# Performance work log

Measured on AMD Instinct MI355X. Metric: run time of the kernel, lower is better.

The kernel has to match this reference:

```python
import jax, jax.numpy as jnp
import numpy as np

B, T = 512, 200
N_SKILLS, M, DK, DV, H = 1000, 50, 64, 64, 128


def setup_inputs() -> dict:
    key = jax.random.key(0)
    ks = jax.random.split(key, 12)
    inp = {
        'skill_seq': jax.random.randint(ks[0], (B, T), 0, N_SKILLS, dtype=jnp.int32),
        'correct_seq': jax.random.randint(ks[1], (B, T), 0, 2, dtype=jnp.int32),
        'mask': jnp.ones((B, T), dtype=jnp.float32),
        'skill_embed': jax.random.normal(ks[2], (N_SKILLS, DK), dtype=jnp.float32),
        'key_memory': jax.random.normal(ks[3], (M, DK), dtype=jnp.float32) * 0.1,
        'value_init': jnp.zeros((M, DV), dtype=jnp.float32),
        'interaction_embed': jax.random.normal(ks[4], (2 * N_SKILLS, DV), dtype=jnp.float32),
        'erase_W': jax.random.normal(ks[5], (DV, DV), dtype=jnp.float32) * 0.05,
        'erase_b': jnp.zeros((DV,), dtype=jnp.float32),
        'add_W': jax.random.normal(ks[6], (DV, DV), dtype=jnp.float32) * 0.05,
        'add_b': jnp.zeros((DV,), dtype=jnp.float32),
        'fc1_W': jax.random.normal(ks[7], (DK + DV, H), dtype=jnp.float32) * 0.05,
        'fc1_b': jnp.zeros((H,), dtype=jnp.float32),
        'fc2_W': jax.random.normal(ks[8], (H, 1), dtype=jnp.float32) * 0.05,
        'fc2_b': jnp.zeros((1,), dtype=jnp.float32),
    }
    return inp


def reference(skill_seq, correct_seq, mask, skill_embed, key_memory, value_init,
              interaction_embed, erase_W, erase_b, add_W, add_b,
              fc1_W, fc1_b, fc2_W, fc2_b):
    n_skills = skill_embed.shape[0]
    b = skill_seq.shape[0]
    # Time-invariant-per-step quantities are precomputed vectorized over (B,T):
    q = skill_embed[skill_seq]                                   # (B,T,dk)
    w = jax.nn.softmax(jnp.einsum('btk,mk->btm', q, key_memory), axis=-1)  # (B,T,M)
    v = interaction_embed[skill_seq + correct_seq * n_skills]    # (B,T,dv)
    e = jax.nn.sigmoid(v @ erase_W + erase_b)                    # (B,T,dv)
    a = jnp.tanh(v @ add_W + add_b)                              # (B,T,dv)

    def step(mem, inputs):
        # mem: (B,M,dv); read BEFORE write, matching the torch loop
        w_t, e_t, a_t = inputs                                   # (B,M),(B,dv),(B,dv)
        read = jnp.einsum('bm,bmv->bv', w_t, mem)                # (B,dv)
        we = w_t[:, :, None]                                     # (B,M,1)
        mem = mem * (1.0 - we * e_t[:, None, :]) + we * a_t[:, None, :]
        return mem, read

    mem0 = jnp.broadcast_to(value_init, (b,) + value_init.shape)
    _, reads = jax.lax.scan(step, mem0,
                            (jnp.swapaxes(w, 0, 1), jnp.swapaxes(e, 0, 1), jnp.swapaxes(a, 0, 1)))
    reads = jnp.swapaxes(reads, 0, 1)                            # (B,T,dv)

    x = jnp.concatenate([q, reads], axis=-1)                     # (B,T,dk+dv)
    h = jax.nn.relu(x @ fc1_W + fc1_b)
    logit = (h @ fc2_W + fc2_b)[..., 0]
    p = jax.nn.sigmoid(logit)
    return p * mask, correct_seq.astype(jnp.float32) * mask
```

## Files before the change

kernel.cpp:

```cpp
#include <hip/hip_runtime.h>
#include <hip/hip_bf16.h>

#define B_  512
#define T_  200
#define NS  1000
#define M_  50
#define DK  64
#define DV  64
#define H_  128
#define NPOS (B_ * T_)

typedef __hip_bfloat16 bf16;
typedef unsigned short ushort_t;
typedef __bf16 bf16x8 __attribute__((ext_vector_type(8)));
typedef float  f32x4  __attribute__((ext_vector_type(4)));

__device__ __forceinline__ float ldf(const void* p, int i, int isbf) {
    return isbf ? __bfloat162float(((const bf16*)p)[i]) : ((const float*)p)[i];
}
__device__ __forceinline__ int sniff(const void* mask) {
    return (*(const unsigned*)mask == 0x3F800000u) ? 0 : 1;
}
__device__ __forceinline__ float rl(float x, int l) {
    return __int_as_float(__builtin_amdgcn_readlane(__float_as_int(x), l));
}
__device__ __forceinline__ ushort_t f2bf(float v) {
    bf16 h = __float2bfloat16(v);
    return *(ushort_t*)&h;
}

__global__ __launch_bounds__(256) void dk21_tabs(
    const void* __restrict__ mask,
    const void* __restrict__ skill_embed, const void* __restrict__ key_memory,
    const void* __restrict__ inter,
    const void* __restrict__ eW, const void* __restrict__ eb,
    const void* __restrict__ aW, const void* __restrict__ ab,
    const void* __restrict__ fc1W, const void* __restrict__ fc1b,
    float* __restrict__ w_tab, unsigned* __restrict__ ea_tab,
    float* __restrict__ hq_tab, ushort_t* __restrict__ W2f) {
    int isbf = sniff(mask);
    int lane = threadIdx.x & 63;
    int gwid = (blockIdx.x << 2) | (threadIdx.x >> 6);

    if (gwid < NS) {
        int s = gwid;
        int kq = lane >> 4, r = lane & 15;
        int row = 13 * kq + r;
        int valid = (r < 13) && (row < M_);
        float q = ldf(skill_embed, s * DK + lane, isbf);
        float acc = 0.f;
        if (valid) {
            #pragma unroll 16
            for (int k = 0; k < DK; ++k)
                acc = fmaf(rl(q, k), ldf(key_memory, row * DK + k, isbf), acc);
        }
        float val = valid ? acc : -1e30f;
        float mx = val;
        #pragma unroll
        for (int off = 1; off < 64; off <<= 1) mx = fmaxf(mx, __shfl_xor(mx, off, 64));
        float ex = valid ? __expf(val - mx) : 0.f;
        float sm = ex;
        #pragma unroll
        for (int off = 1; off < 64; off <<= 1) sm += __shfl_xor(sm, off, 64);
        w_tab[s * 64 + lane] = valid ? ex / sm : 0.f;
    } else if (gwid < 3 * NS) {
        int r = gwid - NS;
        float vv = ldf(inter, r * DV + lane, isbf);
        float eacc = ldf(eb, lane, isbf);
        float aacc = ldf(ab, lane, isbf);
        #pragma unroll 16
        for (int u = 0; u < DV; ++u) {
            float vu = rl(vv, u);
            eacc = fmaf(vu, ldf(eW, u * DV + lane, isbf), eacc);
            aacc = fmaf(vu, ldf(aW, u * DV + lane, isbf), aacc);
        }
        float ev = 1.f / (1.f + __expf(-eacc));
        float av = tanhf(aacc);
        ea_tab[r * 64 + lane] = ((unsigned)f2bf(av) << 16) | (unsigned)f2bf(ev);
    } else if (gwid < 4 * NS) {
        int s = gwid - 3 * NS;
        float q = ldf(skill_embed, s * DK + lane, isbf);
        float acc0 = ldf(fc1b, lane, isbf);
        float acc1 = ldf(fc1b, 64 + lane, isbf);
        #pragma unroll 16
        for (int k = 0; k < DK; ++k) {
            float qk = rl(q, k);
            acc0 = fmaf(qk, ldf(fc1W, k * H_ + lane, isbf), acc0);
            acc1 = fmaf(qk, ldf(fc1W, k * H_ + 64 + lane, isbf), acc1);
        }
        hq_tab[s * H_ + lane]      = acc0;
        hq_tab[s * H_ + 64 + lane] = acc1;
    } else if (gwid < 4 * NS + 16) {
        int f = gwid - 4 * NS;
        int tile = f >> 1, kk = f & 1;
        int n = tile * 16 + (lane & 15);
        #pragma unroll
        for (int j = 0; j < 8; ++j) {
            int v = kk * 32 + (lane >> 4) * 8 + j;
            W2f[(f * 64 + lane) * 8 + j] = f2bf(ldf(fc1W, (DK + v) * H_ + n, isbf));
        }
    }
}

#define SC_STEP(D, TP) { \
    unsigned ea = eas[D]; \
    float e0 = __uint_as_float(ea << 16); \
    float a0 = __uint_as_float(ea & 0xFFFF0000u); \
    float acc0 = 0.f, acc1 = 0.f, acc2 = 0.f, acc3 = 0.f; \
    _Pragma("unroll") \
    for (int i = 0; i < 3; ++i) { \
        float4 w = wst[D][i]; \
        acc0 = fmaf(w.x, mem[i].x, acc0); \
        acc1 = fmaf(w.y, mem[i].y, acc1); \
        acc2 = fmaf(w.z, mem[i].z, acc2); \
        acc3 = fmaf(w.w, mem[i].w, acc3); \
        mem[i].x = fmaf(-w.x, fmaf(e0, mem[i].x, -a0), mem[i].x); \
        mem[i].y = fmaf(-w.y, fmaf(e0, mem[i].y, -a0), mem[i].y); \
        mem[i].z = fmaf(-w.z, fmaf(e0, mem[i].z, -a0), mem[i].z); \
        mem[i].w = fmaf(-w.w, fmaf(e0, mem[i].w, -a0), mem[i].w); \
    } \
    float wS = w3[D]; \
    acc0 = fmaf(wS, memS, acc0); \
    memS = fmaf(-wS, fmaf(e0, memS, -a0), memS); \
    *(ushort_t*)((char*)outp + (TP) * 512) = f2bf((acc0 + acc1) + (acc2 + acc3)); \
    eas[D]    = ea_tab[(sA + cA * NS) * 64 + lane]; \
    wst[D][0] = w4[sA * 16 + 4 * k + 0]; \
    wst[D][1] = w4[sA * 16 + 4 * k + 1]; \
    wst[D][2] = w4[sA * 16 + 4 * k + 2]; \
    w3[D]     = w_tab[sA * 64 + 16 * k + 12]; \
    sA = sB; cA = cB; \
    { int tf_ = tbase + (TP) + 6; tf_ = tf_ < T_ ? tf_ : T_ - 1; \
      sB = ss[base + tf_]; cB = cs[base + tf_]; } }

__global__ __launch_bounds__(64, 2) void dk21_scan(
    const int*  __restrict__ ss, const int* __restrict__ cs,
    const void* __restrict__ mask, const void* __restrict__ value_init,
    const float* __restrict__ w_tab, const unsigned* __restrict__ ea_tab,
    ushort_t* __restrict__ read_bf) {

    int isbf = sniff(mask);
    int lane = threadIdx.x;
    int bk   = blockIdx.x;
    int b    = bk >> 2, k = bk & 3;
    const int base = b * T_;
    const float4* w4 = (const float4*)w_tab;

    float4 mem[3]; float memS;
    #pragma unroll
    for (int i = 0; i < 3; ++i) {
        int r = 13 * k + 4 * i;
        mem[i].x = (r + 0 < M_) ? ldf(value_init, (r + 0) * DV + lane, isbf) : 0.f;
        mem[i].y = (r + 1 < M_) ? ldf(value_init, (r + 1) * DV + lane, isbf) : 0.f;
        mem[i].z = (r + 2 < M_) ? ldf(value_init, (r + 2) * DV + lane, isbf) : 0.f;
        mem[i].w = (r + 3 < M_) ? ldf(value_init, (r + 3) * DV + lane, isbf) : 0.f;
    }
    { int r = 13 * k + 12; memS = (r < M_) ? ldf(value_init, r * DV + lane, isbf) : 0.f; }

    float4   wst[4][3];
    float    w3[4];
    unsigned eas[4];
    #pragma unroll
    for (int d = 0; d < 4; ++d) {
        int s = ss[base + d], c = cs[base + d];
        eas[d]    = ea_tab[(s + c * NS) * 64 + lane];
        wst[d][0] = w4[s * 16 + 4 * k + 0];
        wst[d][1] = w4[s * 16 + 4 * k + 1];
        wst[d][2] = w4[s * 16 + 4 * k + 2];
        w3[d]     = w_tab[s * 64 + 16 * k + 12];
    }
    int sA = ss[base + 4], cA = cs[base + 4];
    int sB = ss[base + 5], cB = cs[base + 5];

    ushort_t* outp = read_bf + ((size_t)base * 4 + k) * 64 + lane;

    for (int cc = 0; cc < 25; ++cc) {
        int tbase = cc * 8;
        SC_STEP(0, 0) SC_STEP(1, 1) SC_STEP(2, 2) SC_STEP(3, 3)
        SC_STEP(0, 4) SC_STEP(1, 5) SC_STEP(2, 6) SC_STEP(3, 7)
        outp += 2048;
    }
}

#define FOR8(X) X(0) X(1) X(2) X(3) X(4) X(5) X(6) X(7)
#define DECL_C(t)  f32x4 c##t = {0.f, 0.f, 0.f, 0.f};
#define LOADB(t) bf16x8 b##t##_0 = B8[(2 * (t)) * 64 + lane], \
                        b##t##_1 = B8[(2 * (t) + 1) * 64 + lane];
#define FCKK(kk, p) { \
    bf16x8 av = A8[col * 32 + (kk) * 4 + quad]; \
    c0 = __builtin_amdgcn_mfma_f32_16x16x32_bf16(av, b0_##p, c0, 0, 0, 0); \
    c1 = __builtin_amdgcn_mfma_f32_16x16x32_bf16(av, b1_##p, c1, 0, 0, 0); \
    c2 = __builtin_amdgcn_mfma_f32_16x16x32_bf16(av, b2_##p, c2, 0, 0, 0); \
    c3 = __builtin_amdgcn_mfma_f32_16x16x32_bf16(av, b3_##p, c3, 0, 0, 0); \
    c4 = __builtin_amdgcn_mfma_f32_16x16x32_bf16(av, b4_##p, c4, 0, 0, 0); \
    c5 = __builtin_amdgcn_mfma_f32_16x16x32_bf16(av, b5_##p, c5, 0, 0, 0); \
    c6 = __builtin_amdgcn_mfma_f32_16x16x32_bf16(av, b6_##p, c6, 0, 0, 0); \
    c7 = __builtin_amdgcn_mfma_f32_16x16x32_bf16(av, b7_##p, c7, 0, 0, 0); }
#define EPI(t) { \
    float h; \
    h = c##t.x + hq_tab[s0r * H_ + t * 16 + col]; x0 = fmaf(fmaxf(h, 0.f), f2w##t, x0); \
    h = c##t.y + hq_tab[s1r * H_ + t * 16 + col]; x1 = fmaf(fmaxf(h, 0.f), f2w##t, x1); \
    h = c##t.z + hq_tab[s2r * H_ + t * 16 + col]; x2 = fmaf(fmaxf(h, 0.f), f2w##t, x2); \
    h = c##t.w + hq_tab[s3r * H_ + t * 16 + col]; x3 = fmaf(fmaxf(h, 0.f), f2w##t, x3); }

__global__ __launch_bounds__(64)
__attribute__((amdgpu_waves_per_eu(3))) void dk21_fc(
    const int*  __restrict__ skill_seq, const int* __restrict__ correct_seq,
    const void* __restrict__ mask,
    const void* __restrict__ fc2W, const void* __restrict__ fc2b,
    const float* __restrict__ hq_tab, const ushort_t* __restrict__ W2f,
    const ushort_t* __restrict__ read_bf,
    float* __restrict__ out0, float* __restrict__ out1) {

    int isbf = sniff(mask);
    int lane = threadIdx.x;
    int col  = lane & 15, quad = lane >> 4;

    const bf16x8* B8 = (const bf16x8*)W2f;
    FOR8(LOADB)

    float f2w0 = ldf(fc2W,   0 + col, isbf), f2w1 = ldf(fc2W,  16 + col, isbf);
    float f2w2 = ldf(fc2W,  32 + col, isbf), f2w3 = ldf(fc2W,  48 + col, isbf);
    float f2w4 = ldf(fc2W,  64 + col, isbf), f2w5 = ldf(fc2W,  80 + col, isbf);
    float f2w6 = ldf(fc2W,  96 + col, isbf), f2w7 = ldf(fc2W, 112 + col, isbf);
    float f2b  = ldf(fc2b, 0, isbf);

    for (int pg = blockIdx.x; pg < NPOS / 16; pg += gridDim.x) {
        int p0 = pg * 16;
        const bf16x8* A8 = (const bf16x8*)(read_bf + (size_t)p0 * 256);

        int s0r = skill_seq[p0 + quad * 4 + 0];
        int s1r = skill_seq[p0 + quad * 4 + 1];
        int s2r = skill_seq[p0 + quad * 4 + 2];
        int s3r = skill_seq[p0 + quad * 4 + 3];

        FOR8(DECL_C)
        FCKK(0, 0) FCKK(1, 1) FCKK(2, 0) FCKK(3, 1)
        FCKK(4, 0) FCKK(5, 1) FCKK(6, 0) FCKK(7, 1)

        float x0 = 0.f, x1 = 0.f, x2 = 0.f, x3 = 0.f;
        FOR8(EPI)

        #pragma unroll
        for (int off = 1; off < 16; off <<= 1) {
            x0 += __shfl_xor(x0, off, 64);
            x1 += __shfl_xor(x1, off, 64);
            x2 += __shfl_xor(x2, off, 64);
            x3 += __shfl_xor(x3, off, 64);
        }

        float mk0 = ldf(mask, p0 + quad * 4 + 0, isbf);
        float mk1 = ldf(mask, p0 + quad * 4 + 1, isbf);
        float mk2 = ldf(mask, p0 + quad * 4 + 2, isbf);
        float mk3 = ldf(mask, p0 + quad * 4 + 3, isbf);
        if (col == 0) {
            out0[p0 + quad * 4 + 0] = mk0 / (1.f + __expf(-(x0 + f2b)));
            out0[p0 + quad * 4 + 1] = mk1 / (1.f + __expf(-(x1 + f2b)));
            out0[p0 + quad * 4 + 2] = mk2 / (1.f + __expf(-(x2 + f2b)));
            out0[p0 + quad * 4 + 3] = mk3 / (1.f + __expf(-(x3 + f2b)));
        }
        if (col == 1) {
            out1[p0 + quad * 4 + 0] = (float)correct_seq[p0 + quad * 4 + 0] * mk0;
            out1[p0 + quad * 4 + 1] = (float)correct_seq[p0 + quad * 4 + 1] * mk1;
            out1[p0 + quad * 4 + 2] = (float)correct_seq[p0 + quad * 4 + 2] * mk2;
            out1[p0 + quad * 4 + 3] = (float)correct_seq[p0 + quad * 4 + 3] * mk3;
        }
    }
}

extern "C" void kernel_launch(void* const* d_in, const int* in_sizes, int n_in,
                              void* d_out, int out_size, void* d_ws, size_t ws_size,
                              hipStream_t stream) {
    const int*  skill_seq   = (const int*)d_in[0];
    const int*  correct_seq = (const int*)d_in[1];
    const void* mask        = d_in[2];
    const void* skill_embed = d_in[3];
    const void* key_memory  = d_in[4];
    const void* value_init  = d_in[5];
    const void* inter       = d_in[6];
    const void* erase_W     = d_in[7];
    const void* erase_b     = d_in[8];
    const void* add_W       = d_in[9];
    const void* add_b       = d_in[10];
    const void* fc1_W       = d_in[11];
    const void* fc1_b       = d_in[12];
    const void* fc2_W       = d_in[13];
    const void* fc2_b       = d_in[14];
    float* out = (float*)d_out;

    float*    ws      = (float*)d_ws + 16;
    float*    w_tab   = ws;
    unsigned* ea_tab  = (unsigned*)(ws + 64000);
    float*    hq_tab  = ws + 192000;
    ushort_t* W2f     = (ushort_t*)(ws + 320000);
    ushort_t* read_bf = (ushort_t*)(ws + 336400);

    dk21_tabs<<<1004, 256, 0, stream>>>(mask, skill_embed, key_memory, inter,
                                        erase_W, erase_b, add_W, add_b,
                                        fc1_W, fc1_b,
                                        w_tab, ea_tab, hq_tab, W2f);

    dk21_scan<<<B_ * 4, 64, 0, stream>>>(skill_seq, correct_seq, mask, value_init,
                                         w_tab, ea_tab, read_bf);

    dk21_fc<<<3200, 64, 0, stream>>>(skill_seq, correct_seq, mask,
                                     fc2_W, fc2_b, hq_tab, W2f, read_bf,
                                     out, out + (size_t)NPOS);
}
```

Baseline: 192.3 us.

## Stage scan gather tables through LDS with async double-buffered global_load_lds

The scan kernel no longer prefetches per-step weight and erase/add rows into registers with a rolling index pipeline. It issues global_load_lds copies for eight steps at a time into a two-buffer shared-memory ring and waits on vmcnt before consuming each chunk. The memory rows are repartitioned from 13 per block to 16 per block, with the w table laid out linearly (lane < 50), which removes the scalar remainder row. This is meant to hide gather latency and cut register pressure. The cost is a manual vmcnt/sched_barrier scheme that relies on the exact count of outstanding loads.

```diff
diff --git a/kernel.cpp b/kernel.cpp
--- a/kernel.cpp
+++ b/kernel.cpp
@@ -29,7 +29,7 @@
     return *(ushort_t*)&h;
 }
 
-__global__ __launch_bounds__(256) void dk21_tabs(
+__global__ __launch_bounds__(256) void dk25_tabs(
     const void* __restrict__ mask,
     const void* __restrict__ skill_embed, const void* __restrict__ key_memory,
     const void* __restrict__ inter,
@@ -44,25 +44,22 @@
 
     if (gwid < NS) {
         int s = gwid;
-        int kq = lane >> 4, r = lane & 15;
-        int row = 13 * kq + r;
-        int valid = (r < 13) && (row < M_);
         float q = ldf(skill_embed, s * DK + lane, isbf);
         float acc = 0.f;
-        if (valid) {
+        if (lane < M_) {
             #pragma unroll 16
             for (int k = 0; k < DK; ++k)
-                acc = fmaf(rl(q, k), ldf(key_memory, row * DK + k, isbf), acc);
-        }
-        float val = valid ? acc : -1e30f;
+                acc = fmaf(rl(q, k), ldf(key_memory, lane * DK + k, isbf), acc);
+        }
+        float val = (lane < M_) ? acc : -1e30f;
         float mx = val;
         #pragma unroll
         for (int off = 1; off < 64; off <<= 1) mx = fmaxf(mx, __shfl_xor(mx, off, 64));
-        float ex = valid ? __expf(val - mx) : 0.f;
+        float ex = (lane < M_) ? __expf(val - mx) : 0.f;
         float sm = ex;
         #pragma unroll
         for (int off = 1; off < 64; off <<= 1) sm += __shfl_xor(sm, off, 64);
-        w_tab[s * 64 + lane] = valid ? ex / sm : 0.f;
+        w_tab[s * 64 + lane] = (lane < M_) ? ex / sm : 0.f;
     } else if (gwid < 3 * NS) {
         int r = gwid - NS;
         float vv = ldf(inter, r * DV + lane, isbf);
@@ -102,82 +99,96 @@
     }
 }
 
-#define SC_STEP(D, TP) { \
-    unsigned ea = eas[D]; \
+
+#define WAITV(N) \
+    asm volatile("s_waitcnt vmcnt(" #N ")" ::: "memory"); \
+    __builtin_amdgcn_sched_barrier(0);
+
+#define GLL(gsrc, ldst) \
+    __builtin_amdgcn_global_load_lds( \
+        (const __attribute__((address_space(1))) void*)(const void*)(gsrc), \
+        (__attribute__((address_space(3))) void*)(void*)(ldst), 4, 0, 0);
+
+#define ISSUE(NB) { \
+    _Pragma("unroll") \
+    for (int st = 0; st < 8; ++st) { \
+        const float*    wsrc_  = w_tab  + sI[st] * 64 + lane; \
+        const unsigned* easrc_ = ea_tab + (sI[st] + cI[st] * NS) * 64 + lane; \
+        GLL(wsrc_,  &ldsw[NB][st][0]) \
+        GLL(easrc_, &ldsea[NB][st][0]) \
+    } }
+
+#define SCROW(W, MEM) \
+    acc0 = fmaf(W.x, MEM.x, acc0); \
+    acc1 = fmaf(W.y, MEM.y, acc1); \
+    acc2 = fmaf(W.z, MEM.z, acc2); \
+    acc3 = fmaf(W.w, MEM.w, acc3); \
+    MEM.x = fmaf(-W.x, fmaf(e0, MEM.x, -a0), MEM.x); \
+    MEM.y = fmaf(-W.y, fmaf(e0, MEM.y, -a0), MEM.y); \
+    MEM.z = fmaf(-W.z, fmaf(e0, MEM.z, -a0), MEM.z); \
+    MEM.w = fmaf(-W.w, fmaf(e0, MEM.w, -a0), MEM.w);
+
+#define PSTEP(NB, TP) { \
+    unsigned ea = ldsea[NB][TP][lane]; \
     float e0 = __uint_as_float(ea << 16); \
     float a0 = __uint_as_float(ea & 0xFFFF0000u); \
     float acc0 = 0.f, acc1 = 0.f, acc2 = 0.f, acc3 = 0.f; \
-    _Pragma("unroll") \
-    for (int i = 0; i < 3; ++i) { \
-        float4 w = wst[D][i]; \
-        acc0 = fmaf(w.x, mem[i].x, acc0); \
-        acc1 = fmaf(w.y, mem[i].y, acc1); \
-        acc2 = fmaf(w.z, mem[i].z, acc2); \
-        acc3 = fmaf(w.w, mem[i].w, acc3); \
-        mem[i].x = fmaf(-w.x, fmaf(e0, mem[i].x, -a0), mem[i].x); \
-        mem[i].y = fmaf(-w.y, fmaf(e0, mem[i].y, -a0), mem[i].y); \
-        mem[i].z = fmaf(-w.z, fmaf(e0, mem[i].z, -a0), mem[i].z); \
-        mem[i].w = fmaf(-w.w, fmaf(e0, mem[i].w, -a0), mem[i].w); \
-    } \
-    float wS = w3[D]; \
-    acc0 = fmaf(wS, memS, acc0); \
-    memS = fmaf(-wS, fmaf(e0, memS, -a0), memS); \
-    *(ushort_t*)((char*)outp + (TP) * 512) = f2bf((acc0 + acc1) + (acc2 + acc3)); \
-    eas[D]    = ea_tab[(sA + cA * NS) * 64 + lane]; \
-    wst[D][0] = w4[sA * 16 + 4 * k + 0]; \
-    wst[D][1] = w4[sA * 16 + 4 * k + 1]; \
-    wst[D][2] = w4[sA * 16 + 4 * k + 2]; \
-    w3[D]     = w_tab[sA * 64 + 16 * k + 12]; \
-    sA = sB; cA = cB; \
-    { int tf_ = tbase + (TP) + 6; tf_ = tf_ < T_ ? tf_ : T_ - 1; \
-      sB = ss[base + tf_]; cB = cs[base + tf_]; } }
-
-__global__ __launch_bounds__(64, 2) void dk21_scan(
+    { float4 w = ldsw[NB][TP][4 * k + 0]; SCROW(w, mem[0]) } \
+    { float4 w = ldsw[NB][TP][4 * k + 1]; SCROW(w, mem[1]) } \
+    { float4 w = ldsw[NB][TP][4 * k + 2]; SCROW(w, mem[2]) } \
+    { float4 w = ldsw[NB][TP][4 * k + 3]; SCROW(w, mem[3]) } \
+    read_bf[outbase + (TP) * 256] = f2bf((acc0 + acc1) + (acc2 + acc3)); }
+
+__global__ __launch_bounds__(64, 2) void dk25_scan(
     const int*  __restrict__ ss, const int* __restrict__ cs,
     const void* __restrict__ mask, const void* __restrict__ value_init,
     const float* __restrict__ w_tab, const unsigned* __restrict__ ea_tab,
     ushort_t* __restrict__ read_bf) {
+
+    __shared__ float4   ldsw[2][8][16];
+    __shared__ unsigned ldsea[2][8][64];
 
     int isbf = sniff(mask);
     int lane = threadIdx.x;
     int bk   = blockIdx.x;
     int b    = bk >> 2, k = bk & 3;
     const int base = b * T_;
-    const float4* w4 = (const float4*)w_tab;
-
-    float4 mem[3]; float memS;
+
+    float4 mem[4];
     #pragma unroll
-    for (int i = 0; i < 3; ++i) {
-        int r = 13 * k + 4 * i;
+    for (int i = 0; i < 4; ++i) {
+        int r = 16 * k + 4 * i;
         mem[i].x = (r + 0 < M_) ? ldf(value_init, (r + 0) * DV + lane, isbf) : 0.f;
         mem[i].y = (r + 1 < M_) ? ldf(value_init, (r + 1) * DV + lane, isbf) : 0.f;
         mem[i].z = (r + 2 < M_) ? ldf(value_init, (r + 2) * DV + lane, isbf) : 0.f;
         mem[i].w = (r + 3 < M_) ? ldf(value_init, (r + 3) * DV + lane, isbf) : 0.f;
     }
-    { int r = 13 * k + 12; memS = (r < M_) ? ldf(value_init, r * DV + lane, isbf) : 0.f; }
-
-    float4   wst[4][3];
-    float    w3[4];
-    unsigned eas[4];
+
+    int sI[8], cI[8];
+
     #pragma unroll
-    for (int d = 0; d < 4; ++d) {
-        int s = ss[base + d], c = cs[base + d];
-        eas[d]    = ea_tab[(s + c * NS) * 64 + lane];
-        wst[d][0] = w4[s * 16 + 4 * k + 0];
-        wst[d][1] = w4[s * 16 + 4 * k + 1];
-        wst[d][2] = w4[s * 16 + 4 * k + 2];
-        w3[d]     = w_tab[s * 64 + 16 * k + 12];
-    }
-    int sA = ss[base + 4], cA = cs[base + 4];
-    int sB = ss[base + 5], cB = cs[base + 5];
-
-    ushort_t* outp = read_bf + ((size_t)base * 4 + k) * 64 + lane;
+    for (int st = 0; st < 8; ++st) { sI[st] = ss[base + st];     cI[st] = cs[base + st]; }
+    ISSUE(0)
+    #pragma unroll
+    for (int st = 0; st < 8; ++st) { sI[st] = ss[base + 8 + st]; cI[st] = cs[base + 8 + st]; }
+    ISSUE(1)
+
+    size_t outbase = ((size_t)base * 4 + k) * 64 + lane;
 
     for (int cc = 0; cc < 25; ++cc) {
-        int tbase = cc * 8;
-        SC_STEP(0, 0) SC_STEP(1, 1) SC_STEP(2, 2) SC_STEP(3, 3)
-        SC_STEP(0, 4) SC_STEP(1, 5) SC_STEP(2, 6) SC_STEP(3, 7)
-        outp += 2048;
+        int nb = cc & 1;
+        int tb2 = 8 * (cc + 2); if (tb2 > T_ - 8) tb2 = T_ - 8;
+        #pragma unroll
+        for (int st = 0; st < 8; ++st) {
+            sI[st] = ss[base + tb2 + st]; cI[st] = cs[base + tb2 + st];
+        }
+        WAITV(16)
+        PSTEP(nb, 0) PSTEP(nb, 1) PSTEP(nb, 2) PSTEP(nb, 3)
+        PSTEP(nb, 4) PSTEP(nb, 5) PSTEP(nb, 6) PSTEP(nb, 7)
+        __builtin_amdgcn_sched_barrier(0);
+        ISSUE(nb)
+        __builtin_amdgcn_sched_barrier(0);
+        outbase += 2048;
     }
 }
 
@@ -203,7 +214,7 @@
     h = c##t.w + hq_tab[s3r * H_ + t * 16 + col]; x3 = fmaf(fmaxf(h, 0.f), f2w##t, x3); }
 
 __global__ __launch_bounds__(64)
-__attribute__((amdgpu_waves_per_eu(3))) void dk21_fc(
+__attribute__((amdgpu_waves_per_eu(3))) void dk25_fc(
     const int*  __restrict__ skill_seq, const int* __restrict__ correct_seq,
     const void* __restrict__ mask,
     const void* __restrict__ fc2W, const void* __restrict__ fc2b,
@@ -294,15 +305,15 @@
     ushort_t* W2f     = (ushort_t*)(ws + 320000);
     ushort_t* read_bf = (ushort_t*)(ws + 336400);
 
-    dk21_tabs<<<1004, 256, 0, stream>>>(mask, skill_embed, key_memory, inter,
+    dk25_tabs<<<1004, 256, 0, stream>>>(mask, skill_embed, key_memory, inter,
                                         erase_W, erase_b, add_W, add_b,
                                         fc1_W, fc1_b,
                                         w_tab, ea_tab, hq_tab, W2f);
 
-    dk21_scan<<<B_ * 4, 64, 0, stream>>>(skill_seq, correct_seq, mask, value_init,
+    dk25_scan<<<B_ * 4, 64, 0, stream>>>(skill_seq, correct_seq, mask, value_init,
                                          w_tab, ea_tab, read_bf);
 
-    dk21_fc<<<3200, 64, 0, stream>>>(skill_seq, correct_seq, mask,
+    dk25_fc<<<3200, 64, 0, stream>>>(skill_seq, correct_seq, mask,
                                      fc2_W, fc2_b, hq_tab, W2f, read_bf,
                                      out, out + (size_t)NPOS);
 }
```

New measurement: 196.0 us. About the same (+1.9%).
